# Optimization experiments

Hardware: AMD Instinct MI355X
Metric: run time of the kernel (lower is better)

## Reference

```python
import jax, jax.numpy as jnp
import numpy as np

LRELU_SLOPE = 0.2
SQRT2 = 1.4142135623730951

def make_coord(h, w):
    # LIIF make_coord: cell-center coords in [-1, 1]; index 0 is the row (dim -2) coord.
    ys = -1.0 + (2.0 * jnp.arange(h, dtype=jnp.float32) + 1.0) / h
    xs = -1.0 + (2.0 * jnp.arange(w, dtype=jnp.float32) + 1.0) / w
    yy, xx = jnp.meshgrid(ys, xs, indexing='ij')
    return jnp.stack([yy, xx], axis=-1).reshape(h * w, 2)  # [Q, 2]

def style_layer(x, style_vec, scale2, shift, mod_w, mod_b, conv_w, act_b):
    # StyleGAN2-style modulated 3x3 conv + instance norm + (scale2, shift) affine + fused leaky relu.
    s = style_vec @ mod_w.T + mod_b                                   # [B, Cin] modulation
    w = conv_w[None] * s[:, None, :, None, None]                      # [B, Cout, Cin, 3, 3]
    demod = jax.lax.rsqrt(jnp.sum(w * w, axis=(2, 3, 4)) + 1e-8)      # [B, Cout]
    y = jax.lax.conv_general_dilated(x * s[:, :, None, None], conv_w, (1, 1), 'SAME',
                                     dimension_numbers=('NCHW', 'OIHW', 'NCHW'))
    y = y * demod[:, :, None, None]
    mu = jnp.mean(y, axis=(2, 3), keepdims=True)
    var = jnp.var(y, axis=(2, 3), keepdims=True)
    y = (y - mu) * jax.lax.rsqrt(var + 1e-5)                          # InstanceNorm2d (no affine)
    y = y * scale2 + shift
    return jax.nn.leaky_relu(y + act_b[None, :, None, None], LRELU_SLOPE) * SQRT2

def reference(x, scale1, scale2, shift, mod_w, mod_b, conv_w, act_b, w1, b1, w2, b2, out_h, out_w):
    B, C, Hf, Wf = x.shape
    feat = style_layer(x, scale1, scale2, shift, mod_w, mod_b, conv_w, act_b)
    Q = out_h * out_w
    coord = jnp.broadcast_to(make_coord(out_h, out_w)[None], (B, Q, 2))  # [B, Q, 2]
    rx = 1.0 / Hf  # = 2/Hf/2
    ry = 1.0 / Wf
    eps_shift = 1e-6
    feat_flat = feat.reshape(B, C, Hf * Wf).transpose(0, 2, 1)  # [B, Hf*Wf, C]
    preds, areas = [], []
    for vx in (-1, 1):
        for vy in (-1, 1):
            cy = jnp.clip(coord[..., 0] + vx * rx + eps_shift, -1.0 + 1e-6, 1.0 - 1e-6)
            cx = jnp.clip(coord[..., 1] + vy * ry + eps_shift, -1.0 + 1e-6, 1.0 - 1e-6)
            # nearest grid_sample (align_corners=False): idx = floor((c+1)/2 * size)
            iy = jnp.clip(jnp.floor((cy + 1.0) * 0.5 * Hf), 0, Hf - 1).astype(jnp.int32)
            ix = jnp.clip(jnp.floor((cx + 1.0) * 0.5 * Wf), 0, Wf - 1).astype(jnp.int32)
            lin = iy * Wf + ix                                        # [B, Q]
            q_feat = jnp.take_along_axis(feat_flat, lin[..., None], axis=1)  # [B, Q, C]
            qy = -1.0 + (2.0 * iy.astype(jnp.float32) + 1.0) / Hf     # nearest feat-cell coord
            qx = -1.0 + (2.0 * ix.astype(jnp.float32) + 1.0) / Wf
            rel_y = (coord[..., 0] - qy) * Hf
            rel_x = (coord[..., 1] - qx) * Wf
            inp = jnp.concatenate([q_feat, rel_y[..., None], rel_x[..., None]], axis=-1)  # [B,Q,C+2]
            pred = (inp @ w1 + b1) @ w2 + b2                          # two stacked Linears, no act
            preds.append(pred)
            areas.append(jnp.abs(rel_y * rel_x) + 1e-9)
    tot_area = areas[0] + areas[1] + areas[2] + areas[3]
    areas = [areas[3], areas[2], areas[1], areas[0]]  # diagonal swap (local ensemble)
    ret = jnp.zeros_like(preds[0])
    for pred, area in zip(preds, areas):
        ret = ret + pred * (area / tot_area)[..., None]
    return ret  # [B, Q, dim]

def setup_inputs() -> dict:
    key = jax.random.key(0)
    ks = jax.random.split(key, 12)
    B, C, Hf, Wf, S = 4, 64, 64, 64, 512
    return {
        'x': jax.random.normal(ks[0], (B, C, Hf, Wf), jnp.float32),
        'scale1': jax.random.normal(ks[1], (B, S), jnp.float32),
        'scale2': jax.random.normal(ks[2], (B, C, 1, 1), jnp.float32),
        'shift': jax.random.normal(ks[3], (B, C, 1, 1), jnp.float32),
        'mod_w': jax.random.normal(ks[4], (C, S), jnp.float32) * 0.02,
        'mod_b': jnp.ones((C,), jnp.float32),
        'conv_w': jax.random.normal(ks[5], (C, C, 3, 3), jnp.float32) * 0.05,
        'act_b': jax.random.normal(ks[6], (C,), jnp.float32) * 0.02,
        'w1': jax.random.normal(ks[7], (C + 2, 256), jnp.float32) * 0.05,
        'b1': jax.random.normal(ks[8], (256,), jnp.float32) * 0.01,
        'w2': jax.random.normal(ks[9], (256, C), jnp.float32) * 0.05,
        'b2': jax.random.normal(ks[10], (C,), jnp.float32) * 0.01,
        'out_h': 256,
        'out_w': 256,
    }
```

## Files before the change

kernel.cpp:

```cpp
#include <hip/hip_runtime.h>

#define SQRT2F 1.41421356237309515f

typedef __attribute__((ext_vector_type(8))) short bf16x8;
typedef __attribute__((ext_vector_type(4))) float f32x4;

enum : int {
  DM_OFF   = 0,
  BC_OFF   = 256,
  WC_OFF   = 1024,
  P_OFF    = 8192,
  Y_OFF    = 65536,
  WS_FLOATS = Y_OFF + 1048576
};

__device__ __align__(16) float WS[WS_FLOATS];

__device__ __forceinline__ unsigned short f2bf(float v) {
  unsigned int u = __float_as_uint(v);
  u += 0x7fffu + ((u >> 16) & 1u);
  return (unsigned short)(u >> 16);
}

__global__ __launch_bounds__(256) void fused1_kernel(
    const float* __restrict__ x,      const float* __restrict__ scale1,
    const float* __restrict__ mod_w,  const float* __restrict__ mod_b,
    const float* __restrict__ conv_w, const float* __restrict__ b1,
    const float* __restrict__ w2,     const float* __restrict__ b2,
    const float* __restrict__ w1) {
  const int bid = blockIdx.x;
  const int t = threadIdx.x;

  __shared__ __align__(16) unsigned short Xl[3 * 66 * 64];
  __shared__ __align__(16) unsigned short Wl[64 * 24 * 8];
  __shared__ float part[256];
  __shared__ float s_sh[64];

  if (bid >= 256) {
    if (bid < 260) {
      const int b = bid - 256;
      const int i = t >> 2, qq = t & 3;
      {
        const float* sv = scale1 + b * 512 + qq * 128;
        const float* mw = mod_w + i * 512 + qq * 128;
        float p = 0.f;
        for (int k = 0; k < 128; ++k) p += sv[k] * mw[k];
        part[t] = p;
      }
      __syncthreads();
      if (qq == 0)
        s_sh[i] = part[t] + part[t + 1] + part[t + 2] + part[t + 3] + mod_b[i];
      __syncthreads();
      {
        const int o = i;
        const float* cw = conv_w + o * 576 + qq * 144;
        float d = 0.f;
        for (int ii = 0; ii < 16; ++ii) {
          float ss = s_sh[qq * 16 + ii];
          float wsq = 0.f;
          #pragma unroll
          for (int k = 0; k < 9; ++k) { float w = cw[ii * 9 + k]; wsq += w * w; }
          d += ss * ss * wsq;
        }
        part[t] = d;
      }
      __syncthreads();
      if (qq == 0)
        WS[DM_OFF + b * 64 + i] =
            rsqrtf(part[t] + part[t + 1] + part[t + 2] + part[t + 3] + 1e-8f);
    } else {
      const int idx = (bid - 260) * 256 + t;
      if (idx < 4224) {
        const int c = idx >> 6, o = idx & 63;
        const float* r1 = w1 + c * 256;
        float acc = 0.f;
        for (int k = 0; k < 256; ++k) acc += r1[k] * w2[k * 64 + o];
        WS[WC_OFF + idx] = acc;
      } else if (idx < 4288) {
        const int o = idx - 4224;
        float a = 0.f;
        for (int k = 0; k < 256; ++k) a += b1[k] * w2[k * 64 + o];
        WS[BC_OFF + o] = a + b2[o];
      }
    }
    return;
  }

  const int b = bid >> 6;
  const int r = bid & 63;
  const int w = t >> 6, lane = t & 63;
  const int l15 = lane & 15, l4 = lane >> 4;

  {
    const int i = t >> 2, qq = t & 3;
    const float* sv = scale1 + b * 512 + qq * 128;
    const float* mw = mod_w + i * 512 + qq * 128;
    float p = 0.f;
    for (int k = 0; k < 128; ++k) p += sv[k] * mw[k];
    part[t] = p;
  }
  __syncthreads();
  if ((t & 3) == 0) {
    const int i = t >> 2;
    s_sh[i] = part[t] + part[t + 1] + part[t + 2] + part[t + 3] + mod_b[i];
  }
  {
    int4* Xz = (int4*)Xl;
    int4 z; z.x = z.y = z.z = z.w = 0;
    for (int idx = t; idx < 1584; idx += 256) Xz[idx] = z;
  }
  __syncthreads();

  {
    const int col = t & 63;
    const int tq = t >> 6;
    unsigned int* Xw = (unsigned int*)Xl;
    for (int it = 0; it < 24; ++it) {
      const int task = it * 4 + tq;
      const int row3 = task >> 5;
      const int ich = (task & 31) * 2;
      const int rr = r - 1 + row3;
      if (rr >= 0 && rr < 64) {
        const float* xb = x + ((size_t)(b * 64 + ich) << 12) + (rr << 6) + col;
        const float v0 = xb[0] * s_sh[ich];
        const float v1 = xb[4096] * s_sh[ich + 1];
        const unsigned int u = (unsigned int)f2bf(v0) | ((unsigned int)f2bf(v1) << 16);
        const int colp = col + 1;
        const int byte = ((row3 * 66 + colp) << 7) + ((((ich >> 3)) ^ (colp & 7)) << 4) + ((ich & 7) << 1);
        Xw[byte >> 2] = u;
      }
    }
  }

  f32x4 acc[4];
  #pragma unroll
  for (int m = 0; m < 4; ++m) acc[m] = (f32x4){0.f, 0.f, 0.f, 0.f};

  const bf16x8* Xv = (const bf16x8*)Xl;
  const bf16x8* Wv = (const bf16x8*)Wl;
  int4* Wst = (int4*)Wl;

  for (int dy = 0; dy < 3; ++dy) {
    __syncthreads();
    for (int i = 0; i < 6; ++i) {
      const int idx = i * 256 + t;
      const int o = idx / 24;
      const int g = idx - o * 24;
      const int dx = g >> 3, gg = g & 7;
      const float* cw = conv_w + o * 576 + (gg * 8) * 9 + dy * 3 + dx;
      int4 v;
      v.x = (int)((unsigned int)f2bf(cw[0])  | ((unsigned int)f2bf(cw[9])  << 16));
      v.y = (int)((unsigned int)f2bf(cw[18]) | ((unsigned int)f2bf(cw[27]) << 16));
      v.z = (int)((unsigned int)f2bf(cw[36]) | ((unsigned int)f2bf(cw[45]) << 16));
      v.w = (int)((unsigned int)f2bf(cw[54]) | ((unsigned int)f2bf(cw[63]) << 16));
      Wst[o * 24 + dx * 8 + (gg ^ (o & 7))] = v;
    }
    __syncthreads();

    #pragma unroll
    for (int dx = 0; dx < 3; ++dx) {
      #pragma unroll
      for (int kh = 0; kh < 2; ++kh) {
        const int kg = kh * 4 + l4;
        bf16x8 afr[4];
        #pragma unroll
        for (int m = 0; m < 4; ++m) {
          const int o = m * 16 + l15;
          afr[m] = Wv[o * 24 + dx * 8 + (kg ^ (o & 7))];
        }
        const int colp = w * 16 + l15 + dx;
        const bf16x8 bfr = Xv[((dy * 66 + colp) << 3) + (kg ^ (colp & 7))];
        #pragma unroll
        for (int m = 0; m < 4; ++m)
          acc[m] = __builtin_amdgcn_mfma_f32_16x16x32_bf16(
              afr[m], bfr, acc[m], 0, 0, 0);
      }
    }
  }

  {
    const int px = w * 16 + l15;
    float* yq = WS + Y_OFF + (((size_t)b * 4096 + r * 64 + px) << 6);
    #pragma unroll
    for (int m = 0; m < 4; ++m)
      *(f32x4*)(yq + m * 16 + l4 * 4) = acc[m];
  }

  __syncthreads();
  float* sred = (float*)Wl;
  {
    #pragma unroll
    for (int m = 0; m < 4; ++m) {
      #pragma unroll
      for (int j = 0; j < 4; ++j) {
        float s1 = acc[m][j];
        float s2 = acc[m][j] * acc[m][j];
        #pragma unroll
        for (int off = 1; off < 16; off <<= 1) {
          s1 += __shfl_xor(s1, off);
          s2 += __shfl_xor(s2, off);
        }
        if (l15 == 0) {
          const int o = m * 16 + l4 * 4 + j;
          sred[(w * 64 + o) * 2 + 0] = s1;
          sred[(w * 64 + o) * 2 + 1] = s2;
        }
      }
    }
  }
  __syncthreads();
  if (t < 128) {
    const int o = t >> 1, wh = t & 1;
    float s = sred[o * 2 + wh] + sred[(64 + o) * 2 + wh] +
              sred[(128 + o) * 2 + wh] + sred[(192 + o) * 2 + wh];
    WS[P_OFF + (((size_t)b * 64 + r) * 64 + o) * 2 + wh] = s;
  }
}

__global__ __launch_bounds__(512) void gout_kernel(
    const float* __restrict__ scale2, const float* __restrict__ shiftp,
    const float* __restrict__ act_b,  float* __restrict__ out) {
  const int bid = blockIdx.x;
  const int b = bid >> 6;
  const int ty = (bid >> 3) & 7;
  const int tx = bid & 7;
  const int t = threadIdx.x;
  const int lane = t & 63;

  __shared__ float A_sh[64], B_sh[64];
  __shared__ float red[1024];
  __shared__ __align__(16) float ft_l[100][68];
  __shared__ __align__(16) float G_l[100][68];

  float wcreg[64];
  #pragma unroll
  for (int c = 0; c < 64; ++c) wcreg[c] = WS[WC_OFF + c * 64 + lane];
  const float bcv = WS[BC_OFF + lane];

  {
    const int c = t & 63, qq = t >> 6;
    const float* p = WS + P_OFF + (((size_t)b * 64 + qq * 8) * 64 + c) * 2;
    float S1 = 0.f, S2 = 0.f;
    #pragma unroll
    for (int rr = 0; rr < 8; ++rr) { S1 += p[rr * 128]; S2 += p[rr * 128 + 1]; }
    red[t] = S1; red[512 + t] = S2;
  }
  __syncthreads();
  if (t < 64) {
    float S1 = 0.f, S2 = 0.f;
    #pragma unroll
    for (int qq = 0; qq < 8; ++qq) { S1 += red[qq * 64 + t]; S2 += red[512 + qq * 64 + t]; }
    const float mu = S1 * (1.f / 4096.f);
    const float var = S2 * (1.f / 4096.f) - mu * mu;
    const float dm = WS[DM_OFF + b * 64 + t];
    const float rstd = rsqrtf(dm * dm * var + 1e-5f);
    const float A = dm * rstd * scale2[b * 64 + t];
    A_sh[t] = A;
    B_sh[t] = -mu * A + shiftp[b * 64 + t] + act_b[t];
  }
  __syncthreads();

  const int cy_base = ty * 8 - 1, cx_base = tx * 8 - 1;
  {
    const float4* A4 = (const float4*)A_sh;
    const float4* B4 = (const float4*)B_sh;
    const float* yb = WS + Y_OFF + ((size_t)b << 18);
    for (int f = t; f < 1600; f += 512) {
      const int cell = f >> 4, cq = f & 15;
      const int li = cell / 10, lj = cell - li * 10;
      const int ciy = cy_base + li, cix = cx_base + lj;
      if (ciy >= 0 && ciy < 64 && cix >= 0 && cix < 64) {
        const float4 y4 = *(const float4*)(yb + (((ciy << 6) + cix) << 6) + cq * 4);
        const float4 Av = A4[cq], Bv = B4[cq];
        float4 fv;
        float u;
        u = y4.x * Av.x + Bv.x; fv.x = (u > 0.f ? u : 0.2f * u) * SQRT2F;
        u = y4.y * Av.y + Bv.y; fv.y = (u > 0.f ? u : 0.2f * u) * SQRT2F;
        u = y4.z * Av.z + Bv.z; fv.z = (u > 0.f ? u : 0.2f * u) * SQRT2F;
        u = y4.w * Av.w + Bv.w; fv.w = (u > 0.f ? u : 0.2f * u) * SQRT2F;
        *(float4*)&ft_l[cell][cq * 4] = fv;
      }
    }
  }
  __syncthreads();

  {
    const int w = t >> 6;
    #pragma unroll
    for (int p = 0; p < 4; ++p) {
      const int cb = p * 32 + w * 4;
      if (cb < 100) {
        #pragma unroll
        for (int i2 = 0; i2 < 4; ++i2) {
          float a = bcv;
          const float* fr = ft_l[cb + i2];
          #pragma unroll
          for (int c = 0; c < 64; c += 4) {
            const float4 fv = *(const float4*)&fr[c];
            a = fmaf(fv.x, wcreg[c], a);
            a = fmaf(fv.y, wcreg[c + 1], a);
            a = fmaf(fv.z, wcreg[c + 2], a);
            a = fmaf(fv.w, wcreg[c + 3], a);
          }
          G_l[cb + i2][lane] = a;
        }
      }
    }
  }

  const int sub = t & 3, chb = sub * 16;
  float4 wa[4], wb[4];
  #pragma unroll
  for (int k = 0; k < 4; ++k) {
    wa[k] = *(const float4*)(WS + WC_OFF + 64 * 64 + chb + k * 4);
    wb[k] = *(const float4*)(WS + WC_OFF + 65 * 64 + chb + k * 4);
  }
  __syncthreads();

  const float lo = -1.f + 1e-6f, hi = 1.f - 1e-6f;
  #pragma unroll 1
  for (int pass = 0; pass < 8; ++pass) {
    const int qi = pass * 128 + (t >> 2);
    const int oy = (ty << 5) + (qi >> 5), ox = (tx << 5) + (qi & 31);

    const float cy0 = -1.f + (2.f * oy + 1.f) * (1.f / 256.f);
    const float cx0 = -1.f + (2.f * ox + 1.f) * (1.f / 256.f);

    int lcell[4];
    float area[4], rely[4], relx[4];
    int j = 0;
    #pragma unroll
    for (int vx = -1; vx <= 1; vx += 2) {
      #pragma unroll
      for (int vy = -1; vy <= 1; vy += 2) {
        float cy = cy0 + (float)vx * (1.f / 64.f) + 1e-6f;
        cy = fminf(fmaxf(cy, lo), hi);
        float cx = cx0 + (float)vy * (1.f / 64.f) + 1e-6f;
        cx = fminf(fmaxf(cx, lo), hi);
        const float fy = floorf((cy + 1.f) * 32.f);
        const float fx = floorf((cx + 1.f) * 32.f);
        const int iy = (int)fminf(fmaxf(fy, 0.f), 63.f);
        const int ix = (int)fminf(fmaxf(fx, 0.f), 63.f);
        const float qy = -1.f + (2.f * iy + 1.f) * (1.f / 64.f);
        const float qx = -1.f + (2.f * ix + 1.f) * (1.f / 64.f);
        const float ry_ = (cy0 - qy) * 64.f;
        const float rx_ = (cx0 - qx) * 64.f;
        lcell[j] = (iy - cy_base) * 10 + (ix - cx_base);
        rely[j] = ry_; relx[j] = rx_;
        area[j] = fabsf(ry_ * rx_) + 1e-9f;
        ++j;
      }
    }
    const float tot = area[0] + area[1] + area[2] + area[3];
    float wgt[4];
    #pragma unroll
    for (int k = 0; k < 4; ++k) wgt[k] = area[3 - k] / tot;
    const float swy = wgt[0] * rely[0] + wgt[1] * rely[1] + wgt[2] * rely[2] + wgt[3] * rely[3];
    const float swx = wgt[0] * relx[0] + wgt[1] * relx[1] + wgt[2] * relx[2] + wgt[3] * relx[3];

    float4 r[4];
    #pragma unroll
    for (int k = 0; k < 4; ++k) {
      r[k].x = swy * wa[k].x + swx * wb[k].x;
      r[k].y = swy * wa[k].y + swx * wb[k].y;
      r[k].z = swy * wa[k].z + swx * wb[k].z;
      r[k].w = swy * wa[k].w + swx * wb[k].w;
    }
    #pragma unroll
    for (int jj = 0; jj < 4; ++jj) {
      const float4* gp = (const float4*)&G_l[lcell[jj]][chb];
      const float wv = wgt[jj];
      #pragma unroll
      for (int k = 0; k < 4; ++k) {
        const float4 gv = gp[k];
        r[k].x += wv * gv.x; r[k].y += wv * gv.y;
        r[k].z += wv * gv.z; r[k].w += wv * gv.w;
      }
    }
    const size_t gq = ((size_t)b << 16) + (oy << 8) + ox;
    float4* op = (float4*)(out + (gq << 6) + chb);
    #pragma unroll
    for (int k = 0; k < 4; ++k) op[k] = r[k];
  }
}

extern "C" void kernel_launch(void* const* d_in, const int* in_sizes, int n_in,
                              void* d_out, int out_size, void* d_ws, size_t ws_size,
                              hipStream_t stream) {
  (void)in_sizes; (void)n_in; (void)out_size; (void)d_ws; (void)ws_size;
  const float* x      = (const float*)d_in[0];
  const float* scale1 = (const float*)d_in[1];
  const float* scale2 = (const float*)d_in[2];
  const float* shiftp = (const float*)d_in[3];
  const float* mod_w  = (const float*)d_in[4];
  const float* mod_b  = (const float*)d_in[5];
  const float* conv_w = (const float*)d_in[6];
  const float* act_b  = (const float*)d_in[7];
  const float* w1     = (const float*)d_in[8];
  const float* b1     = (const float*)d_in[9];
  const float* w2     = (const float*)d_in[10];
  const float* b2     = (const float*)d_in[11];
  float* out = (float*)d_out;

  hipLaunchKernelGGL(fused1_kernel, dim3(277), dim3(256), 0, stream,
                     x, scale1, mod_w, mod_b, conv_w, b1, w2, b2, w1);
  hipLaunchKernelGGL(gout_kernel, dim3(256), dim3(512), 0, stream,
                     scale2, shiftp, act_b, out);
}
```

Before: 70.16 us.

## Merge conv and gather kernels into one persistent kernel with per-batch grid barrier

Fuses the modulated-conv kernel and the LIIF gather/output kernel into a single 256-block, 512-thread launch. A per-batch global atomic barrier replaces the kernel boundary, so the demod and weight-product side work is folded into the first few blocks of each batch. Shared memory for the two phases is overlaid through a union. The MFMA work is split across 8 waves, with each wave handling 32 output channels for 16 pixels. This removes one launch and the tail gap between kernels, but it depends on all 64 blocks of a batch being co-resident, otherwise the barrier deadlocks. It also adds spin-wait overhead.

```diff
diff --git a/kernel.cpp b/kernel.cpp
--- a/kernel.cpp
+++ b/kernel.cpp
@@ -15,6 +15,22 @@
 };
 
 __device__ __align__(16) float WS[WS_FLOATS];
+__device__ unsigned bar_cnt[4];
+__device__ unsigned bar_gen[4];
+
+struct ConvSh {
+  unsigned short Xl[3 * 66 * 64];
+  unsigned short Wl[64 * 24 * 8];
+  float part[512];
+  float s_sh[64];
+};
+struct GoutSh {
+  float ft[100][68];
+  float G[100][68];
+  float red[1024];
+  float A[64], B[64];
+};
+union ShU { ConvSh c; GoutSh g; };
 
 __device__ __forceinline__ unsigned short f2bf(float v) {
   unsigned int u = __float_as_uint(v);
@@ -22,60 +38,75 @@
   return (unsigned short)(u >> 16);
 }
 
-__global__ __launch_bounds__(256) void fused1_kernel(
+__global__ __launch_bounds__(512, 2) void mega_kernel(
     const float* __restrict__ x,      const float* __restrict__ scale1,
+    const float* __restrict__ scale2, const float* __restrict__ shiftp,
     const float* __restrict__ mod_w,  const float* __restrict__ mod_b,
-    const float* __restrict__ conv_w, const float* __restrict__ b1,
-    const float* __restrict__ w2,     const float* __restrict__ b2,
-    const float* __restrict__ w1) {
+    const float* __restrict__ conv_w, const float* __restrict__ act_b,
+    const float* __restrict__ b1,     const float* __restrict__ w2,
+    const float* __restrict__ b2,     const float* __restrict__ w1,
+    float* __restrict__ out) {
   const int bid = blockIdx.x;
+  const int b = bid >> 6;
+  const int r = bid & 63;
   const int t = threadIdx.x;
-
-  __shared__ __align__(16) unsigned short Xl[3 * 66 * 64];
-  __shared__ __align__(16) unsigned short Wl[64 * 24 * 8];
-  __shared__ float part[256];
-  __shared__ float s_sh[64];
-
-  if (bid >= 256) {
-    if (bid < 260) {
-      const int b = bid - 256;
-      const int i = t >> 2, qq = t & 3;
-      {
-        const float* sv = scale1 + b * 512 + qq * 128;
-        const float* mw = mod_w + i * 512 + qq * 128;
-        float p = 0.f;
-        for (int k = 0; k < 128; ++k) p += sv[k] * mw[k];
-        part[t] = p;
-      }
-      __syncthreads();
-      if (qq == 0)
-        s_sh[i] = part[t] + part[t + 1] + part[t + 2] + part[t + 3] + mod_b[i];
-      __syncthreads();
-      {
-        const int o = i;
-        const float* cw = conv_w + o * 576 + qq * 144;
-        float d = 0.f;
-        for (int ii = 0; ii < 16; ++ii) {
-          float ss = s_sh[qq * 16 + ii];
-          float wsq = 0.f;
-          #pragma unroll
-          for (int k = 0; k < 9; ++k) { float w = cw[ii * 9 + k]; wsq += w * w; }
-          d += ss * ss * wsq;
-        }
-        part[t] = d;
-      }
-      __syncthreads();
-      if (qq == 0)
-        WS[DM_OFF + b * 64 + i] =
-            rsqrtf(part[t] + part[t + 1] + part[t + 2] + part[t + 3] + 1e-8f);
-    } else {
-      const int idx = (bid - 260) * 256 + t;
+  const int w = t >> 6, lane = t & 63;
+  const int l15 = lane & 15, l4 = lane >> 4;
+
+  __shared__ __align__(16) ShU sh;
+
+  {
+    const int i = t >> 3, qq = t & 7;
+    const float* sv = scale1 + b * 512 + qq * 64;
+    const float* mw = mod_w + i * 512 + qq * 64;
+    float p = 0.f;
+    for (int k = 0; k < 64; ++k) p += sv[k] * mw[k];
+    sh.c.part[t] = p;
+  }
+  __syncthreads();
+  if ((t & 7) == 0) {
+    const int i = t >> 3;
+    float s = mod_b[i];
+    #pragma unroll
+    for (int k = 0; k < 8; ++k) s += sh.c.part[t + k];
+    sh.c.s_sh[i] = s;
+  }
+  __syncthreads();
+
+  if (r == 0) {
+    const int o = t >> 3, qq = t & 7;
+    const float* cw = conv_w + o * 576 + qq * 72;
+    float d = 0.f;
+    #pragma unroll
+    for (int ii = 0; ii < 8; ++ii) {
+      const float ss = sh.c.s_sh[qq * 8 + ii];
+      float wsq = 0.f;
+      #pragma unroll
+      for (int k = 0; k < 9; ++k) { const float wv = cw[ii * 9 + k]; wsq += wv * wv; }
+      d += ss * ss * wsq;
+    }
+    sh.c.part[t] = d;
+    __syncthreads();
+    if ((t & 7) == 0) {
+      float dd = 1e-8f;
+      #pragma unroll
+      for (int k = 0; k < 8; ++k) dd += sh.c.part[t + k];
+      WS[DM_OFF + b * 64 + (t >> 3)] = rsqrtf(dd);
+    }
+    __syncthreads();
+  }
+
+  if (r >= 1 && r <= 4) {
+    const int q = r - 1;
+    #pragma unroll
+    for (int rep = 0; rep < 3; ++rep) {
+      const int idx = q * 512 + t + rep * 2048;
       if (idx < 4224) {
         const int c = idx >> 6, o = idx & 63;
         const float* r1 = w1 + c * 256;
-        float acc = 0.f;
-        for (int k = 0; k < 256; ++k) acc += r1[k] * w2[k * 64 + o];
-        WS[WC_OFF + idx] = acc;
+        float a = 0.f;
+        for (int k = 0; k < 256; ++k) a += r1[k] * w2[k * 64 + o];
+        WS[WC_OFF + idx] = a;
       } else if (idx < 4288) {
         const int o = idx - 4224;
         float a = 0.f;
@@ -83,47 +114,28 @@
         WS[BC_OFF + o] = a + b2[o];
       }
     }
-    return;
-  }
-
-  const int b = bid >> 6;
-  const int r = bid & 63;
-  const int w = t >> 6, lane = t & 63;
-  const int l15 = lane & 15, l4 = lane >> 4;
-
-  {
-    const int i = t >> 2, qq = t & 3;
-    const float* sv = scale1 + b * 512 + qq * 128;
-    const float* mw = mod_w + i * 512 + qq * 128;
-    float p = 0.f;
-    for (int k = 0; k < 128; ++k) p += sv[k] * mw[k];
-    part[t] = p;
-  }
-  __syncthreads();
-  if ((t & 3) == 0) {
-    const int i = t >> 2;
-    s_sh[i] = part[t] + part[t + 1] + part[t + 2] + part[t + 3] + mod_b[i];
-  }
-  {
-    int4* Xz = (int4*)Xl;
+  }
+
+  {
+    int4* Xz = (int4*)sh.c.Xl;
     int4 z; z.x = z.y = z.z = z.w = 0;
-    for (int idx = t; idx < 1584; idx += 256) Xz[idx] = z;
+    for (int idx = t; idx < 1584; idx += 512) Xz[idx] = z;
   }
   __syncthreads();
 
   {
     const int col = t & 63;
     const int tq = t >> 6;
-    unsigned int* Xw = (unsigned int*)Xl;
-    for (int it = 0; it < 24; ++it) {
-      const int task = it * 4 + tq;
+    unsigned int* Xw = (unsigned int*)sh.c.Xl;
+    for (int it = 0; it < 12; ++it) {
+      const int task = it * 8 + tq;
       const int row3 = task >> 5;
       const int ich = (task & 31) * 2;
       const int rr = r - 1 + row3;
       if (rr >= 0 && rr < 64) {
         const float* xb = x + ((size_t)(b * 64 + ich) << 12) + (rr << 6) + col;
-        const float v0 = xb[0] * s_sh[ich];
-        const float v1 = xb[4096] * s_sh[ich + 1];
+        const float v0 = xb[0] * sh.c.s_sh[ich];
+        const float v1 = xb[4096] * sh.c.s_sh[ich + 1];
         const unsigned int u = (unsigned int)f2bf(v0) | ((unsigned int)f2bf(v1) << 16);
         const int colp = col + 1;
         const int byte = ((row3 * 66 + colp) << 7) + ((((ich >> 3)) ^ (colp & 7)) << 4) + ((ich & 7) << 1);
@@ -132,18 +144,20 @@
     }
   }
 
-  f32x4 acc[4];
-  #pragma unroll
-  for (int m = 0; m < 4; ++m) acc[m] = (f32x4){0.f, 0.f, 0.f, 0.f};
-
-  const bf16x8* Xv = (const bf16x8*)Xl;
-  const bf16x8* Wv = (const bf16x8*)Wl;
-  int4* Wst = (int4*)Wl;
+  const int oh = w >> 2, pg = w & 3;
+  f32x4 acc[2];
+  acc[0] = (f32x4){0.f, 0.f, 0.f, 0.f};
+  acc[1] = (f32x4){0.f, 0.f, 0.f, 0.f};
+
+  const bf16x8* Xv = (const bf16x8*)sh.c.Xl;
+  const bf16x8* Wv = (const bf16x8*)sh.c.Wl;
+  int4* Wst = (int4*)sh.c.Wl;
 
   for (int dy = 0; dy < 3; ++dy) {
     __syncthreads();
-    for (int i = 0; i < 6; ++i) {
-      const int idx = i * 256 + t;
+    #pragma unroll
+    for (int i = 0; i < 3; ++i) {
+      const int idx = i * 512 + t;
       const int o = idx / 24;
       const int g = idx - o * 24;
       const int dx = g >> 3, gg = g & 7;
@@ -162,16 +176,16 @@
       #pragma unroll
       for (int kh = 0; kh < 2; ++kh) {
         const int kg = kh * 4 + l4;
-        bf16x8 afr[4];
+        bf16x8 afr[2];
         #pragma unroll
-        for (int m = 0; m < 4; ++m) {
-          const int o = m * 16 + l15;
+        for (int m = 0; m < 2; ++m) {
+          const int o = oh * 32 + m * 16 + l15;
           afr[m] = Wv[o * 24 + dx * 8 + (kg ^ (o & 7))];
         }
-        const int colp = w * 16 + l15 + dx;
+        const int colp = pg * 16 + l15 + dx;
         const bf16x8 bfr = Xv[((dy * 66 + colp) << 3) + (kg ^ (colp & 7))];
         #pragma unroll
-        for (int m = 0; m < 4; ++m)
+        for (int m = 0; m < 2; ++m)
           acc[m] = __builtin_amdgcn_mfma_f32_16x16x32_bf16(
               afr[m], bfr, acc[m], 0, 0, 0);
       }
@@ -179,18 +193,18 @@
   }
 
   {
-    const int px = w * 16 + l15;
+    const int px = pg * 16 + l15;
     float* yq = WS + Y_OFF + (((size_t)b * 4096 + r * 64 + px) << 6);
     #pragma unroll
-    for (int m = 0; m < 4; ++m)
-      *(f32x4*)(yq + m * 16 + l4 * 4) = acc[m];
-  }
-
-  __syncthreads();
-  float* sred = (float*)Wl;
-  {
-    #pragma unroll
-    for (int m = 0; m < 4; ++m) {
+    for (int m = 0; m < 2; ++m)
+      *(f32x4*)(yq + oh * 32 + m * 16 + l4 * 4) = acc[m];
+  }
+
+  __syncthreads();
+  {
+    float* sred = sh.c.part;
+    #pragma unroll
+    for (int m = 0; m < 2; ++m) {
       #pragma unroll
       for (int j = 0; j < 4; ++j) {
         float s1 = acc[m][j];
@@ -201,36 +215,47 @@
           s2 += __shfl_xor(s2, off);
         }
         if (l15 == 0) {
-          const int o = m * 16 + l4 * 4 + j;
-          sred[(w * 64 + o) * 2 + 0] = s1;
-          sred[(w * 64 + o) * 2 + 1] = s2;
+          const int ol = m * 16 + l4 * 4 + j;
+          sred[(w * 32 + ol) * 2 + 0] = s1;
+          sred[(w * 32 + ol) * 2 + 1] = s2;
         }
       }
     }
-  }
-  __syncthreads();
-  if (t < 128) {
-    const int o = t >> 1, wh = t & 1;
-    float s = sred[o * 2 + wh] + sred[(64 + o) * 2 + wh] +
-              sred[(128 + o) * 2 + wh] + sred[(192 + o) * 2 + wh];
-    WS[P_OFF + (((size_t)b * 64 + r) * 64 + o) * 2 + wh] = s;
-  }
-}
-
-__global__ __launch_bounds__(512) void gout_kernel(
-    const float* __restrict__ scale2, const float* __restrict__ shiftp,
-    const float* __restrict__ act_b,  float* __restrict__ out) {
-  const int bid = blockIdx.x;
-  const int b = bid >> 6;
+    __syncthreads();
+    if (t < 128) {
+      const int o = t >> 1, wh = t & 1;
+      const int ohh = o >> 5, ol = o & 31;
+      float s = 0.f;
+      #pragma unroll
+      for (int pq = 0; pq < 4; ++pq)
+        s += sred[(((ohh * 4 + pq) * 32) + ol) * 2 + wh];
+      WS[P_OFF + (((size_t)b * 64 + r) * 64 + o) * 2 + wh] = s;
+    }
+  }
+
+  __syncthreads();
+  if (t == 0) {
+    const unsigned gen = __hip_atomic_load(&bar_gen[b], __ATOMIC_RELAXED,
+                                           __HIP_MEMORY_SCOPE_AGENT);
+    __threadfence();
+    const unsigned old = __hip_atomic_fetch_add(&bar_cnt[b], 1u, __ATOMIC_ACQ_REL,
+                                                __HIP_MEMORY_SCOPE_AGENT);
+    if (old == 63u) {
+      __hip_atomic_store(&bar_cnt[b], 0u, __ATOMIC_RELAXED,
+                         __HIP_MEMORY_SCOPE_AGENT);
+      __hip_atomic_fetch_add(&bar_gen[b], 1u, __ATOMIC_RELEASE,
+                             __HIP_MEMORY_SCOPE_AGENT);
+    } else {
+      while (__hip_atomic_load(&bar_gen[b], __ATOMIC_ACQUIRE,
+                               __HIP_MEMORY_SCOPE_AGENT) == gen)
+        __builtin_amdgcn_s_sleep(2);
+    }
+    __threadfence();
+  }
+  __syncthreads();
+
   const int ty = (bid >> 3) & 7;
   const int tx = bid & 7;
-  const int t = threadIdx.x;
-  const int lane = t & 63;
-
-  __shared__ float A_sh[64], B_sh[64];
-  __shared__ float red[1024];
-  __shared__ __align__(16) float ft_l[100][68];
-  __shared__ __align__(16) float G_l[100][68];
 
   float wcreg[64];
   #pragma unroll
@@ -243,27 +268,30 @@
     float S1 = 0.f, S2 = 0.f;
     #pragma unroll
     for (int rr = 0; rr < 8; ++rr) { S1 += p[rr * 128]; S2 += p[rr * 128 + 1]; }
-    red[t] = S1; red[512 + t] = S2;
+    sh.g.red[t] = S1; sh.g.red[512 + t] = S2;
   }
   __syncthreads();
   if (t < 64) {
     float S1 = 0.f, S2 = 0.f;
     #pragma unroll
-    for (int qq = 0; qq < 8; ++qq) { S1 += red[qq * 64 + t]; S2 += red[512 + qq * 64 + t]; }
+    for (int qq = 0; qq < 8; ++qq) {
+      S1 += sh.g.red[qq * 64 + t];
+      S2 += sh.g.red[512 + qq * 64 + t];
+    }
     const float mu = S1 * (1.f / 4096.f);
     const float var = S2 * (1.f / 4096.f) - mu * mu;
     const float dm = WS[DM_OFF + b * 64 + t];
     const float rstd = rsqrtf(dm * dm * var + 1e-5f);
     const float A = dm * rstd * scale2[b * 64 + t];
-    A_sh[t] = A;
-    B_sh[t] = -mu * A + shiftp[b * 64 + t] + act_b[t];
+    sh.g.A[t] = A;
+    sh.g.B[t] = -mu * A + shiftp[b * 64 + t] + act_b[t];
   }
   __syncthreads();
 
   const int cy_base = ty * 8 - 1, cx_base = tx * 8 - 1;
   {
-    const float4* A4 = (const float4*)A_sh;
-    const float4* B4 = (const float4*)B_sh;
+    const float4* A4 = (const float4*)sh.g.A;
+    const float4* B4 = (const float4*)sh.g.B;
     const float* yb = WS + Y_OFF + ((size_t)b << 18);
     for (int f = t; f < 1600; f += 512) {
       const int cell = f >> 4, cq = f & 15;
@@ -278,14 +306,13 @@
         u = y4.y * Av.y + Bv.y; fv.y = (u > 0.f ? u : 0.2f * u) * SQRT2F;
         u = y4.z * Av.z + Bv.z; fv.z = (u > 0.f ? u : 0.2f * u) * SQRT2F;
         u = y4.w * Av.w + Bv.w; fv.w = (u > 0.f ? u : 0.2f * u) * SQRT2F;
-        *(float4*)&ft_l[cell][cq * 4] = fv;
-      }
-    }
-  }
-  __syncthreads();
-
-  {
-    const int w = t >> 6;
+        *(float4*)&sh.g.ft[cell][cq * 4] = fv;
+      }
+    }
+  }
+  __syncthreads();
+
+  {
     #pragma unroll
     for (int p = 0; p < 4; ++p) {
       const int cb = p * 32 + w * 4;
@@ -293,7 +320,7 @@
         #pragma unroll
         for (int i2 = 0; i2 < 4; ++i2) {
           float a = bcv;
-          const float* fr = ft_l[cb + i2];
+          const float* fr = sh.g.ft[cb + i2];
           #pragma unroll
           for (int c = 0; c < 64; c += 4) {
             const float4 fv = *(const float4*)&fr[c];
@@ -302,7 +329,7 @@
             a = fmaf(fv.z, wcreg[c + 2], a);
             a = fmaf(fv.w, wcreg[c + 3], a);
           }
-          G_l[cb + i2][lane] = a;
+          sh.g.G[cb + i2][lane] = a;
         }
       }
     }
@@ -358,29 +385,29 @@
     const float swy = wgt[0] * rely[0] + wgt[1] * rely[1] + wgt[2] * rely[2] + wgt[3] * rely[3];
     const float swx = wgt[0] * relx[0] + wgt[1] * relx[1] + wgt[2] * relx[2] + wgt[3] * relx[3];
 
-    float4 r[4];
+    float4 rr[4];
     #pragma unroll
     for (int k = 0; k < 4; ++k) {
-      r[k].x = swy * wa[k].x + swx * wb[k].x;
-      r[k].y = swy * wa[k].y + swx * wb[k].y;
-      r[k].z = swy * wa[k].z + swx * wb[k].z;
-      r[k].w = swy * wa[k].w + swx * wb[k].w;
+      rr[k].x = swy * wa[k].x + swx * wb[k].x;
+      rr[k].y = swy * wa[k].y + swx * wb[k].y;
+      rr[k].z = swy * wa[k].z + swx * wb[k].z;
+      rr[k].w = swy * wa[k].w + swx * wb[k].w;
     }
     #pragma unroll
     for (int jj = 0; jj < 4; ++jj) {
-      const float4* gp = (const float4*)&G_l[lcell[jj]][chb];
+      const float4* gp = (const float4*)&sh.g.G[lcell[jj]][chb];
       const float wv = wgt[jj];
       #pragma unroll
       for (int k = 0; k < 4; ++k) {
         const float4 gv = gp[k];
-        r[k].x += wv * gv.x; r[k].y += wv * gv.y;
-        r[k].z += wv * gv.z; r[k].w += wv * gv.w;
+        rr[k].x += wv * gv.x; rr[k].y += wv * gv.y;
+        rr[k].z += wv * gv.z; rr[k].w += wv * gv.w;
       }
     }
     const size_t gq = ((size_t)b << 16) + (oy << 8) + ox;
     float4* op = (float4*)(out + (gq << 6) + chb);
     #pragma unroll
-    for (int k = 0; k < 4; ++k) op[k] = r[k];
+    for (int k = 0; k < 4; ++k) op[k] = rr[k];
   }
 }
 
@@ -402,8 +429,7 @@
   const float* b2     = (const float*)d_in[11];
   float* out = (float*)d_out;
 
-  hipLaunchKernelGGL(fused1_kernel, dim3(277), dim3(256), 0, stream,
-                     x, scale1, mod_w, mod_b, conv_w, b1, w2, b2, w1);
-  hipLaunchKernelGGL(gout_kernel, dim3(256), dim3(512), 0, stream,
-                     scale2, shiftp, act_b, out);
+  hipLaunchKernelGGL(mega_kernel, dim3(256), dim3(512), 0, stream,
+                     x, scale1, scale2, shiftp, mod_w, mod_b, conv_w, act_b,
+                     b1, w2, b2, w1, out);
 }
```

Result: slower. 195.9 us (+179.2%).
